# Optimization experiments

Measured on AMD Instinct MI355X. Metric: run time of the kernel, lower is better.

The kernel has to match this reference:

```python
import jax, jax.numpy as jnp
import numpy as np

N_NODES = 50000
N_EDGES = 1600000
D = 128
N_GRAPHS = 64


def gcn_conv(x, row, col, deg_inv_sqrt, W, b):
    # GCNConv: out_i = sum_{j->i} norm_ij * (x_j @ W) + norm_ii * (x_i @ W) + b
    # with self-loops folded in and norm_ij = d_i^{-1/2} d_j^{-1/2}
    h = x @ W  # [N, H]
    norm = deg_inv_sqrt[row] * deg_inv_sqrt[col]  # [E]
    msg = h[row] * norm[:, None]  # gather over source nodes
    agg = jax.ops.segment_sum(msg, col, num_segments=N_NODES)
    agg = agg + h * (deg_inv_sqrt * deg_inv_sqrt)[:, None]  # self-loop term
    return agg + b


def setup_inputs() -> dict:
    key = jax.random.key(0)
    ks = jax.random.split(key, 12)
    x = jax.random.normal(ks[0], (N_NODES, D), dtype=jnp.float32)
    edge_index = jax.random.randint(ks[1], (2, N_EDGES), 0, N_NODES, dtype=jnp.int32)
    batch = jnp.sort(jax.random.randint(ks[2], (N_NODES,), 0, N_GRAPHS, dtype=jnp.int32))
    s = 1.0 / np.sqrt(D)
    W1 = jax.random.uniform(ks[3], (D, D), jnp.float32, -s, s)
    b1 = jax.random.uniform(ks[4], (D,), jnp.float32, -s, s)
    W2 = jax.random.uniform(ks[5], (D, D), jnp.float32, -s, s)
    b2 = jax.random.uniform(ks[6], (D,), jnp.float32, -s, s)
    W3 = jax.random.uniform(ks[7], (D, D), jnp.float32, -s, s)
    b3 = jax.random.uniform(ks[8], (D,), jnp.float32, -s, s)
    Wf = jax.random.uniform(ks[9], (D, 1), jnp.float32, -s, s)
    bf = jax.random.uniform(ks[10], (1,), jnp.float32, -s, s)
    return {"x": x, "edge_index": edge_index, "batch": batch,
            "W1": W1, "b1": b1, "W2": W2, "b2": b2, "W3": W3, "b3": b3,
            "Wf": Wf, "bf": bf}


def reference(x, edge_index, batch, W1, b1, W2, b2, W3, b3, Wf, bf):
    row, col = edge_index[0], edge_index[1]  # source -> target
    ones = jnp.ones((N_EDGES,), dtype=jnp.float32)
    deg = jax.ops.segment_sum(ones, col, num_segments=N_NODES) + 1.0  # +1 self-loop
    deg_inv_sqrt = jax.lax.rsqrt(deg)

    h = x
    for W, b in ((W1, b1), (W2, b2), (W3, b3)):
        h = gcn_conv(h, row, col, deg_inv_sqrt, W, b)
        h = jax.nn.relu(h)  # dropout is identity in eval mode (p=0)

    # global mean pool over graphs
    sums = jax.ops.segment_sum(h, batch, num_segments=N_GRAPHS)
    counts = jax.ops.segment_sum(jnp.ones((N_NODES,), jnp.float32), batch, num_segments=N_GRAPHS)
    pooled = sums / jnp.maximum(counts, 1.0)[:, None]  # [G, D]

    out = pooled @ Wf + bf  # [G, 1]
    return jax.nn.sigmoid(out)
```

## Files before the change

kernel.cpp:

```cpp
#include <hip/hip_runtime.h>
#include <hip/hip_fp16.h>
#include <math.h>

#define N_NODES 50000
#define N_EDGES 1600000
#define DIM     128
#define N_GRAPHS 64

typedef unsigned int uint32;
typedef __attribute__((ext_vector_type(8))) short bf16x8;
typedef __attribute__((ext_vector_type(4))) float f32x4;

static __device__ __forceinline__ ushort f2b(float f) {
    uint32 u = __float_as_uint(f);
    uint32 r = (u + 0x7fffu + ((u >> 16) & 1u)) >> 16;
    return (ushort)r;
}
static __device__ __forceinline__ float b2f(ushort h) {
    return __uint_as_float(((uint32)h) << 16);
}
static __device__ __forceinline__ unsigned char f2e5(float f) {
    ushort hb = __half_as_ushort(__float2half(f));
    return (unsigned char)(((uint32)hb + 0x7fu + ((hb >> 8) & 1u)) >> 8);
}
union h2u_t { uint32 u; __half2 h; };
static __device__ __forceinline__ __half2 u2h2(uint32 u) { h2u_t t; t.u = u; return t.h; }
static __device__ __forceinline__ __half2 dec01(uint32 v) {
    return u2h2(__builtin_amdgcn_perm(v, 0u, 0x05000400u));
}

#define NBUK 196
#define CAP  16384
#define PB1  400
#define CHUNK1 (N_EDGES / PB1)

__global__ void initg_k(int* __restrict__ gfill) {
    int t = threadIdx.x;
    if (t < NBUK) gfill[t] = t * CAP;
}

__global__ __launch_bounds__(256) void bin_k(const int* __restrict__ col,
                                             const int* __restrict__ row,
                                             int* __restrict__ gfill,
                                             uint32* __restrict__ packed) {
    __shared__ int hist[NBUK];
    __shared__ int cur[NBUK];
    int tid = threadIdx.x;
    for (int t = tid; t < NBUK; t += 256) hist[t] = 0;
    __syncthreads();
    int start = blockIdx.x * CHUNK1, end = start + CHUNK1;
    for (int e = start + tid; e < end; e += 256)
        atomicAdd(&hist[col[e] >> 8], 1);
    __syncthreads();
    for (int t = tid; t < NBUK; t += 256) {
        int h = hist[t];
        cur[t] = h ? atomicAdd(&gfill[t], h) : 0;
    }
    __syncthreads();
    for (int e = start + tid; e < end; e += 256) {
        int c = col[e];
        int r = row[e];
        int pos = atomicAdd(&cur[c >> 8], 1);
        packed[pos] = ((uint32)(c & 255) << 16) | (uint32)r;
    }
}

__global__ void bscan_k(const int* __restrict__ gfill, int* __restrict__ bbase) {
    __shared__ int sm[256];
    int t = threadIdx.x;
    int v = (t < NBUK) ? (gfill[t] - t * CAP) : 0;
    sm[t] = v;
    __syncthreads();
    for (int off = 1; off < 256; off <<= 1) {
        int u = 0;
        if (t >= off) u = sm[t - off];
        __syncthreads();
        if (t >= off) sm[t] += u;
        __syncthreads();
    }
    if (t < NBUK) bbase[t] = sm[t] - v;
}

__global__ __launch_bounds__(256) void bucket_k(const uint32* __restrict__ packed,
                                                const int* __restrict__ gfill,
                                                const int* __restrict__ bbase,
                                                int* __restrict__ cnt,
                                                int* __restrict__ offs,
                                                float* __restrict__ dis,
                                                int* __restrict__ csr) {
    __shared__ int hist[256];
    __shared__ int sm[256];
    __shared__ int lo[256];
    __shared__ int rank[256];
    int b = blockIdx.x, tid = threadIdx.x;
    int size = gfill[b] - b * CAP;
    const uint32* pk = packed + (size_t)b * CAP;
    hist[tid] = 0; rank[tid] = 0;
    __syncthreads();
    for (int e = tid; e < size; e += 256) atomicAdd(&hist[pk[e] >> 16], 1);
    __syncthreads();
    int h = hist[tid];
    sm[tid] = h;
    __syncthreads();
    for (int off = 1; off < 256; off <<= 1) {
        int u = 0;
        if (tid >= off) u = sm[tid - off];
        __syncthreads();
        if (tid >= off) sm[tid] += u;
        __syncthreads();
    }
    lo[tid] = sm[tid] - h;
    int gb = bbase[b];
    int node = (b << 8) + tid;
    if (node < N_NODES) {
        cnt[node]  = h;
        offs[node] = gb + lo[tid];
        dis[node]  = rsqrtf((float)h + 1.0f);
    }
    __syncthreads();
    for (int e = tid; e < size; e += 256) {
        uint32 p = pk[e];
        int cl = p >> 16;
        int r = atomicAdd(&rank[cl], 1);
        csr[gb + lo[cl] + r] = (int)(p & 0xffffu);
    }
}

__global__ __launch_bounds__(256) void conv_k(const float* __restrict__ x, ushort* __restrict__ xb) {
    int i = blockIdx.x * blockDim.x + threadIdx.x;
    const int n4 = N_NODES * DIM / 4;
    if (i >= n4) return;
    float4 v = ((const float4*)x)[i];
    ushort4 o;
    o.x = f2b(v.x); o.y = f2b(v.y); o.z = f2b(v.z); o.w = f2b(v.w);
    ((ushort4*)xb)[i] = o;
}

__global__ __launch_bounds__(256) void wtr_k(const float* __restrict__ W, ushort* __restrict__ wt) {
    int t = blockIdx.x * 256 + threadIdx.x;
    int n = t >> 7, k = t & 127;
    wt[n * 128 + k] = f2b(W[k * 128 + n]);
}

__global__ __launch_bounds__(256) void gemm_mfma_k(const ushort* __restrict__ xb,
                                                   const ushort* __restrict__ wt,
                                                   const float* __restrict__ dis,
                                                   unsigned char* __restrict__ gb) {
    int wid  = threadIdx.x >> 6;
    int lane = threadIdx.x & 63;
    int r0 = blockIdx.x * 64 + wid * 16;
    int m  = lane & 15;
    int kg = lane >> 4;

    int arow = r0 + m;
    if (arow >= N_NODES) arow = N_NODES - 1;
    const ushort* abase = xb + (size_t)arow * DIM + kg * 8;
    const ushort* wbase = wt + (size_t)m * DIM + kg * 8;

    f32x4 acc[8];
    #pragma unroll
    for (int nt = 0; nt < 8; ++nt) acc[nt] = (f32x4){0.f, 0.f, 0.f, 0.f};

    #pragma unroll
    for (int kb = 0; kb < 4; ++kb) {
        bf16x8 a = *(const bf16x8*)(abase + kb * 32);
        #pragma unroll
        for (int nt = 0; nt < 8; ++nt) {
            bf16x8 b = *(const bf16x8*)(wbase + (size_t)nt * 16 * DIM + kb * 32);
            acc[nt] = __builtin_amdgcn_mfma_f32_16x16x32_bf16(a, b, acc[nt], 0, 0, 0);
        }
    }

    int orow0 = r0 + kg * 4;
    float dsc[4];
    #pragma unroll
    for (int i = 0; i < 4; ++i) {
        int rr = orow0 + i;
        dsc[i] = (rr < N_NODES) ? dis[rr] : 0.f;
    }
    #pragma unroll
    for (int i = 0; i < 4; ++i) {
        int rr = orow0 + i;
        if (rr >= N_NODES) continue;
        unsigned char* orow = gb + (size_t)rr * DIM + m;
        #pragma unroll
        for (int nt = 0; nt < 8; ++nt)
            orow[nt * 16] = f2e5(acc[nt][i] * dsc[i]);
    }
}

__global__ __launch_bounds__(256) void agg_k(const unsigned char* __restrict__ gb,
                                             const float* __restrict__ dis,
                                             const int* __restrict__ csr,
                                             const int* __restrict__ offs,
                                             const int* __restrict__ cnt,
                                             const float* __restrict__ bias,
                                             ushort* __restrict__ outb) {
    int lane = threadIdx.x & 63;
    int node = blockIdx.x * 4 + (threadIdx.x >> 6);
    if (node >= N_NODES) return;
    const unsigned char* gl = gb + ((uint32)lane << 1);

    uint32 sv = *(const ushort*)(gl + ((uint32)node << 7));
    __half2 a0 = dec01(sv);
    __half2 a1 = u2h2(0), a2 = u2h2(0), a3 = u2h2(0);

    int base = offs[node];
    int c = cnt[node];
    for (int s0 = 0; s0 < c; s0 += 64) {
        int rem = c - s0;
        int m = rem < 64 ? rem : 64;
        int idx = 0;
        if (lane < m) idx = csr[base + s0 + lane];
        int t = 0;
        for (; t + 8 <= m; t += 8) {
            int j0 = __shfl(idx, t, 64),     j1 = __shfl(idx, t + 1, 64);
            int j2 = __shfl(idx, t + 2, 64), j3 = __shfl(idx, t + 3, 64);
            int j4 = __shfl(idx, t + 4, 64), j5 = __shfl(idx, t + 5, 64);
            int j6 = __shfl(idx, t + 6, 64), j7 = __shfl(idx, t + 7, 64);
            uint32 v0 = *(const ushort*)(gl + ((uint32)j0 << 7));
            uint32 v1 = *(const ushort*)(gl + ((uint32)j1 << 7));
            uint32 v2 = *(const ushort*)(gl + ((uint32)j2 << 7));
            uint32 v3 = *(const ushort*)(gl + ((uint32)j3 << 7));
            uint32 v4 = *(const ushort*)(gl + ((uint32)j4 << 7));
            uint32 v5 = *(const ushort*)(gl + ((uint32)j5 << 7));
            uint32 v6 = *(const ushort*)(gl + ((uint32)j6 << 7));
            uint32 v7 = *(const ushort*)(gl + ((uint32)j7 << 7));
            a0 = __hadd2(a0, dec01(v0));
            a1 = __hadd2(a1, dec01(v1));
            a2 = __hadd2(a2, dec01(v2));
            a3 = __hadd2(a3, dec01(v3));
            a0 = __hadd2(a0, dec01(v4));
            a1 = __hadd2(a1, dec01(v5));
            a2 = __hadd2(a2, dec01(v6));
            a3 = __hadd2(a3, dec01(v7));
        }
        for (; t < m; ++t) {
            int j = __shfl(idx, t, 64);
            uint32 v = *(const ushort*)(gl + ((uint32)j << 7));
            a0 = __hadd2(a0, dec01(v));
        }
    }

    __half2 acc = __hadd2(__hadd2(a0, a1), __hadd2(a2, a3));
    float f0 = __low2float(acc), f1 = __high2float(acc);
    float d = dis[node];
    float bx = bias[lane * 2], by = bias[lane * 2 + 1];
    float ox = fmaxf(fmaf(f0, d, bx), 0.f);
    float oy = fmaxf(fmaf(f1, d, by), 0.f);
    uint32 pk = (uint32)f2b(ox) | ((uint32)f2b(oy) << 16);
    *(uint32*)(outb + ((size_t)node << 7) + ((uint32)lane << 1)) = pk;
}

#define POOL_BLOCKS 512
__global__ __launch_bounds__(128) void pool_k(const ushort* __restrict__ hb,
                                              const int* __restrict__ batch,
                                              float* __restrict__ pooled,
                                              float* __restrict__ counts) {
    const int chunk = (N_NODES + POOL_BLOCKS - 1) / POOL_BLOCKS;
    int tid = threadIdx.x;
    int start = blockIdx.x * chunk;
    int end = start + chunk; if (end > N_NODES) end = N_NODES;
    if (start >= end) return;

    float acc = 0.f;
    int cur = batch[start];
    int cl = 0;
    for (int n = start; n < end; ++n) {
        int b = batch[n];
        if (b != cur) {
            atomicAdd(&pooled[cur * DIM + tid], acc);
            if (tid == 0) atomicAdd(&counts[cur], (float)cl);
            acc = 0.f; cl = 0; cur = b;
        }
        acc += b2f(hb[((size_t)n << 7) + tid]);
        ++cl;
    }
    atomicAdd(&pooled[cur * DIM + tid], acc);
    if (tid == 0) atomicAdd(&counts[cur], (float)cl);
}

__global__ void final_k(const float* __restrict__ pooled, const float* __restrict__ counts,
                        const float* __restrict__ Wf, const float* __restrict__ bf,
                        float* __restrict__ out) {
    __shared__ float sred[2];
    int gidx = blockIdx.x;
    int tid = threadIdx.x;
    float c = fmaxf(counts[gidx], 1.0f);
    float v = pooled[gidx * DIM + tid] / c * Wf[tid];
    for (int off = 32; off > 0; off >>= 1) v += __shfl_down(v, off, 64);
    if ((tid & 63) == 0) sred[tid >> 6] = v;
    __syncthreads();
    if (tid == 0) {
        float t = sred[0] + sred[1] + bf[0];
        out[gidx] = 1.0f / (1.0f + expf(-t));
    }
}

extern "C" void kernel_launch(void* const* d_in, const int* in_sizes, int n_in,
                              void* d_out, int out_size, void* d_ws, size_t ws_size,
                              hipStream_t stream) {
    const float* x     = (const float*)d_in[0];
    const int*   ei    = (const int*)d_in[1];
    const int*   batch = (const int*)d_in[2];
    const float* W1 = (const float*)d_in[3];  const float* b1 = (const float*)d_in[4];
    const float* W2 = (const float*)d_in[5];  const float* b2 = (const float*)d_in[6];
    const float* W3 = (const float*)d_in[7];  const float* b3 = (const float*)d_in[8];
    const float* Wf = (const float*)d_in[9];  const float* bf = (const float*)d_in[10];
    const int* rowp = ei;
    const int* colp = ei + N_EDGES;

    char* ws = (char*)d_ws;
    size_t o = 0;
    auto alloc = [&](size_t bytes) -> void* {
        void* p = ws + o;
        o += (bytes + 255) & ~(size_t)255;
        return p;
    };
    int*    cnt    = (int*)   alloc((size_t)N_NODES * 4);
    int*    offs   = (int*)   alloc((size_t)N_NODES * 4);
    int*    gfill  = (int*)   alloc(256 * 4);
    int*    bbase  = (int*)   alloc(256 * 4);
    float*  dis    = (float*) alloc((size_t)N_NODES * 4);
    int*    csr    = (int*)   alloc((size_t)N_EDGES * 4);
    uint32* packed = (uint32*)alloc((size_t)NBUK * CAP * 4);
    float*  pooled = (float*) alloc((size_t)(N_GRAPHS * DIM + N_GRAPHS) * 4);
    ushort* wt     = (ushort*)alloc((size_t)DIM * DIM * 2);
    unsigned char* bufA = (unsigned char*)alloc((size_t)N_NODES * DIM);
    ushort* bufB   = (ushort*)alloc((size_t)N_NODES * DIM * 2);
    float*  counts = pooled + N_GRAPHS * DIM;

    hipMemsetAsync(pooled, 0, (size_t)(N_GRAPHS * DIM + N_GRAPHS) * 4, stream);

    initg_k<<<1, 256, 0, stream>>>(gfill);
    bin_k<<<PB1, 256, 0, stream>>>(colp, rowp, gfill, packed);
    bscan_k<<<1, 256, 0, stream>>>(gfill, bbase);
    bucket_k<<<NBUK, 256, 0, stream>>>(packed, gfill, bbase, cnt, offs, dis, csr);

    conv_k<<<(N_NODES * DIM / 4 + 255) / 256, 256, 0, stream>>>(x, bufB);

    const int GB = (N_NODES + 63) / 64;

    wtr_k<<<64, 256, 0, stream>>>(W1, wt);
    gemm_mfma_k<<<GB, 256, 0, stream>>>(bufB, wt, dis, bufA);
    agg_k<<<(N_NODES + 3) / 4, 256, 0, stream>>>(bufA, dis, csr, offs, cnt, b1, bufB);
    wtr_k<<<64, 256, 0, stream>>>(W2, wt);
    gemm_mfma_k<<<GB, 256, 0, stream>>>(bufB, wt, dis, bufA);
    agg_k<<<(N_NODES + 3) / 4, 256, 0, stream>>>(bufA, dis, csr, offs, cnt, b2, bufB);
    wtr_k<<<64, 256, 0, stream>>>(W3, wt);
    gemm_mfma_k<<<GB, 256, 0, stream>>>(bufB, wt, dis, bufA);
    agg_k<<<(N_NODES + 3) / 4, 256, 0, stream>>>(bufA, dis, csr, offs, cnt, b3, bufB);

    pool_k<<<POOL_BLOCKS, 128, 0, stream>>>(bufB, batch, pooled, counts);
    final_k<<<N_GRAPHS, 128, 0, stream>>>(pooled, counts, Wf, bf, (float*)d_out);
}
```

Baseline: 282.6 us.

## Merge prep kernels, fold bucket scan, shrink CSR to u16, widen GEMM tiles

Merges the three weight transposes and the gfill init into a single prep kernel, which removes several launches. The separate bucket-base scan kernel is dropped and each bucket block now redoes that scan redundantly. The CSR source indices are stored as 16-bit values to halve index traffic in aggregation, and each GEMM wave now computes 32 rows so every B fragment load is reused twice. Storing indices in 16 bits is only safe if source ids fit in 16 bits; with 50000 nodes they do (below 65536), and the packed format already relied on this.

```diff
diff --git a/kernel.cpp b/kernel.cpp
--- a/kernel.cpp
+++ b/kernel.cpp
@@ -34,9 +34,23 @@
 #define PB1  400
 #define CHUNK1 (N_EDGES / PB1)
 
-__global__ void initg_k(int* __restrict__ gfill) {
-    int t = threadIdx.x;
-    if (t < NBUK) gfill[t] = t * CAP;
+__global__ __launch_bounds__(256) void prep_k(const float* __restrict__ W1,
+                                              const float* __restrict__ W2,
+                                              const float* __restrict__ W3,
+                                              ushort* __restrict__ wt,
+                                              int* __restrict__ gfill) {
+    int blk = blockIdx.x;
+    if (blk < 192) {
+        int w = blk >> 6;
+        const float* W = (w == 0) ? W1 : (w == 1) ? W2 : W3;
+        ushort* o = wt + w * (DIM * DIM);
+        int t = (blk & 63) * 256 + threadIdx.x;
+        int n = t >> 7, k = t & 127;
+        o[n * 128 + k] = f2b(W[k * 128 + n]);
+    } else {
+        int t = threadIdx.x;
+        if (t < NBUK) gfill[t] = t * CAP;
+    }
 }
 
 __global__ __launch_bounds__(256) void bin_k(const int* __restrict__ col,
@@ -65,35 +79,32 @@
     }
 }
 
-__global__ void bscan_k(const int* __restrict__ gfill, int* __restrict__ bbase) {
-    __shared__ int sm[256];
-    int t = threadIdx.x;
-    int v = (t < NBUK) ? (gfill[t] - t * CAP) : 0;
-    sm[t] = v;
-    __syncthreads();
-    for (int off = 1; off < 256; off <<= 1) {
-        int u = 0;
-        if (t >= off) u = sm[t - off];
-        __syncthreads();
-        if (t >= off) sm[t] += u;
-        __syncthreads();
-    }
-    if (t < NBUK) bbase[t] = sm[t] - v;
-}
-
 __global__ __launch_bounds__(256) void bucket_k(const uint32* __restrict__ packed,
                                                 const int* __restrict__ gfill,
-                                                const int* __restrict__ bbase,
                                                 int* __restrict__ cnt,
                                                 int* __restrict__ offs,
                                                 float* __restrict__ dis,
-                                                int* __restrict__ csr) {
+                                                ushort* __restrict__ csr) {
+    __shared__ int bsm[256];
     __shared__ int hist[256];
     __shared__ int sm[256];
     __shared__ int lo[256];
     __shared__ int rank[256];
     int b = blockIdx.x, tid = threadIdx.x;
+
+    int bsz = (tid < NBUK) ? (gfill[tid] - tid * CAP) : 0;
+    bsm[tid] = bsz;
+    __syncthreads();
+    for (int off = 1; off < 256; off <<= 1) {
+        int u = 0;
+        if (tid >= off) u = bsm[tid - off];
+        __syncthreads();
+        if (tid >= off) bsm[tid] += u;
+        __syncthreads();
+    }
     int size = gfill[b] - b * CAP;
+    int gb = bsm[b] - size;
+
     const uint32* pk = packed + (size_t)b * CAP;
     hist[tid] = 0; rank[tid] = 0;
     __syncthreads();
@@ -110,7 +121,6 @@
         __syncthreads();
     }
     lo[tid] = sm[tid] - h;
-    int gb = bbase[b];
     int node = (b << 8) + tid;
     if (node < N_NODES) {
         cnt[node]  = h;
@@ -122,7 +132,7 @@
         uint32 p = pk[e];
         int cl = p >> 16;
         int r = atomicAdd(&rank[cl], 1);
-        csr[gb + lo[cl] + r] = (int)(p & 0xffffu);
+        csr[gb + lo[cl] + r] = (ushort)(p & 0xffffu);
     }
 }
 
@@ -136,62 +146,61 @@
     ((ushort4*)xb)[i] = o;
 }
 
-__global__ __launch_bounds__(256) void wtr_k(const float* __restrict__ W, ushort* __restrict__ wt) {
-    int t = blockIdx.x * 256 + threadIdx.x;
-    int n = t >> 7, k = t & 127;
-    wt[n * 128 + k] = f2b(W[k * 128 + n]);
-}
-
 __global__ __launch_bounds__(256) void gemm_mfma_k(const ushort* __restrict__ xb,
                                                    const ushort* __restrict__ wt,
                                                    const float* __restrict__ dis,
                                                    unsigned char* __restrict__ gb) {
     int wid  = threadIdx.x >> 6;
     int lane = threadIdx.x & 63;
-    int r0 = blockIdx.x * 64 + wid * 16;
+    int r0 = blockIdx.x * 128 + wid * 32;
     int m  = lane & 15;
     int kg = lane >> 4;
 
-    int arow = r0 + m;
-    if (arow >= N_NODES) arow = N_NODES - 1;
-    const ushort* abase = xb + (size_t)arow * DIM + kg * 8;
-    const ushort* wbase = wt + (size_t)m * DIM + kg * 8;
-
-    f32x4 acc[8];
+    int arow0 = r0 + m;
+    int arow1 = r0 + 16 + m;
+    if (arow0 >= N_NODES) arow0 = N_NODES - 1;
+    if (arow1 >= N_NODES) arow1 = N_NODES - 1;
+    const ushort* abase0 = xb + (size_t)arow0 * DIM + kg * 8;
+    const ushort* abase1 = xb + (size_t)arow1 * DIM + kg * 8;
+    const ushort* wbase  = wt + (size_t)m * DIM + kg * 8;
+
+    f32x4 acc[2][8];
     #pragma unroll
-    for (int nt = 0; nt < 8; ++nt) acc[nt] = (f32x4){0.f, 0.f, 0.f, 0.f};
+    for (int hh = 0; hh < 2; ++hh)
+        #pragma unroll
+        for (int nt = 0; nt < 8; ++nt) acc[hh][nt] = (f32x4){0.f, 0.f, 0.f, 0.f};
 
     #pragma unroll
     for (int kb = 0; kb < 4; ++kb) {
-        bf16x8 a = *(const bf16x8*)(abase + kb * 32);
+        bf16x8 a0 = *(const bf16x8*)(abase0 + kb * 32);
+        bf16x8 a1 = *(const bf16x8*)(abase1 + kb * 32);
         #pragma unroll
         for (int nt = 0; nt < 8; ++nt) {
             bf16x8 b = *(const bf16x8*)(wbase + (size_t)nt * 16 * DIM + kb * 32);
-            acc[nt] = __builtin_amdgcn_mfma_f32_16x16x32_bf16(a, b, acc[nt], 0, 0, 0);
-        }
-    }
-
-    int orow0 = r0 + kg * 4;
-    float dsc[4];
+            acc[0][nt] = __builtin_amdgcn_mfma_f32_16x16x32_bf16(a0, b, acc[0][nt], 0, 0, 0);
+            acc[1][nt] = __builtin_amdgcn_mfma_f32_16x16x32_bf16(a1, b, acc[1][nt], 0, 0, 0);
+        }
+    }
+
     #pragma unroll
-    for (int i = 0; i < 4; ++i) {
-        int rr = orow0 + i;
-        dsc[i] = (rr < N_NODES) ? dis[rr] : 0.f;
-    }
-    #pragma unroll
-    for (int i = 0; i < 4; ++i) {
-        int rr = orow0 + i;
-        if (rr >= N_NODES) continue;
-        unsigned char* orow = gb + (size_t)rr * DIM + m;
+    for (int hh = 0; hh < 2; ++hh) {
+        int orow0 = r0 + hh * 16 + kg * 4;
         #pragma unroll
-        for (int nt = 0; nt < 8; ++nt)
-            orow[nt * 16] = f2e5(acc[nt][i] * dsc[i]);
+        for (int i = 0; i < 4; ++i) {
+            int rr = orow0 + i;
+            if (rr >= N_NODES) continue;
+            float dsc = dis[rr];
+            unsigned char* orow = gb + (size_t)rr * DIM + m;
+            #pragma unroll
+            for (int nt = 0; nt < 8; ++nt)
+                orow[nt * 16] = f2e5(acc[hh][nt][i] * dsc);
+        }
     }
 }
 
 __global__ __launch_bounds__(256) void agg_k(const unsigned char* __restrict__ gb,
                                              const float* __restrict__ dis,
-                                             const int* __restrict__ csr,
+                                             const ushort* __restrict__ csr,
                                              const int* __restrict__ offs,
                                              const int* __restrict__ cnt,
                                              const float* __restrict__ bias,
@@ -320,35 +329,30 @@
     int*    cnt    = (int*)   alloc((size_t)N_NODES * 4);
     int*    offs   = (int*)   alloc((size_t)N_NODES * 4);
     int*    gfill  = (int*)   alloc(256 * 4);
-    int*    bbase  = (int*)   alloc(256 * 4);
     float*  dis    = (float*) alloc((size_t)N_NODES * 4);
-    int*    csr    = (int*)   alloc((size_t)N_EDGES * 4);
+    ushort* csr    = (ushort*)alloc((size_t)N_EDGES * 2);
     uint32* packed = (uint32*)alloc((size_t)NBUK * CAP * 4);
     float*  pooled = (float*) alloc((size_t)(N_GRAPHS * DIM + N_GRAPHS) * 4);
-    ushort* wt     = (ushort*)alloc((size_t)DIM * DIM * 2);
+    ushort* wt     = (ushort*)alloc((size_t)3 * DIM * DIM * 2);
     unsigned char* bufA = (unsigned char*)alloc((size_t)N_NODES * DIM);
     ushort* bufB   = (ushort*)alloc((size_t)N_NODES * DIM * 2);
     float*  counts = pooled + N_GRAPHS * DIM;
 
     hipMemsetAsync(pooled, 0, (size_t)(N_GRAPHS * DIM + N_GRAPHS) * 4, stream);
 
-    initg_k<<<1, 256, 0, stream>>>(gfill);
+    prep_k<<<193, 256, 0, stream>>>(W1, W2, W3, wt, gfill);
     bin_k<<<PB1, 256, 0, stream>>>(colp, rowp, gfill, packed);
-    bscan_k<<<1, 256, 0, stream>>>(gfill, bbase);
-    bucket_k<<<NBUK, 256, 0, stream>>>(packed, gfill, bbase, cnt, offs, dis, csr);
+    bucket_k<<<NBUK, 256, 0, stream>>>(packed, gfill, cnt, offs, dis, csr);
 
     conv_k<<<(N_NODES * DIM / 4 + 255) / 256, 256, 0, stream>>>(x, bufB);
 
-    const int GB = (N_NODES + 63) / 64;
-
-    wtr_k<<<64, 256, 0, stream>>>(W1, wt);
+    const int GB = (N_NODES + 127) / 128;
+
     gemm_mfma_k<<<GB, 256, 0, stream>>>(bufB, wt, dis, bufA);
     agg_k<<<(N_NODES + 3) / 4, 256, 0, stream>>>(bufA, dis, csr, offs, cnt, b1, bufB);
-    wtr_k<<<64, 256, 0, stream>>>(W2, wt);
-    gemm_mfma_k<<<GB, 256, 0, stream>>>(bufB, wt, dis, bufA);
+    gemm_mfma_k<<<GB, 256, 0, stream>>>(bufB, wt + DIM * DIM, dis, bufA);
     agg_k<<<(N_NODES + 3) / 4, 256, 0, stream>>>(bufA, dis, csr, offs, cnt, b2, bufB);
-    wtr_k<<<64, 256, 0, stream>>>(W3, wt);
-    gemm_mfma_k<<<GB, 256, 0, stream>>>(bufB, wt, dis, bufA);
+    gemm_mfma_k<<<GB, 256, 0, stream>>>(bufB, wt + 2 * DIM * DIM, dis, bufA);
     agg_k<<<(N_NODES + 3) / 4, 256, 0, stream>>>(bufA, dis, csr, offs, cnt, b3, bufB);
 
     pool_k<<<POOL_BLOCKS, 128, 0, stream>>>(bufB, batch, pooled, counts);
```

Result: faster. 258.4 us (-8.5%).
